# Kernel tuning notes

Measured on AMD Instinct MI355X. Metric: run time of the kernel, lower is better.

## Reference

```python
import jax, jax.numpy as jnp
import numpy as np

TOP_K = 2

def setup_inputs() -> dict:
    key = jax.random.key(0)
    kx, kg, k1, k2 = jax.random.split(key, 4)
    B, T, D, E, H = 4, 1024, 1024, 8, 2048
    x = jax.random.normal(kx, (B, T, D), dtype=jnp.float32)
    Wg = jax.random.normal(kg, (D, E), dtype=jnp.float32) * 0.02
    W1 = jax.random.normal(k1, (E, D, H), dtype=jnp.float32) * 0.02  # c_fc per expert
    W2 = jax.random.normal(k2, (E, H, D), dtype=jnp.float32) * 0.02  # c_proj per expert
    return {"x": x, "Wg": Wg, "W1": W1, "W2": W2}

def reference(x, Wg, W1, W2):
    B, T, D = x.shape
    E = W1.shape[0]
    # Router: softmax over experts, top-k, renormalize top-k weights
    logits = jnp.einsum('btd,de->bte', x, Wg)          # (B,T,E)
    probs = jax.nn.softmax(logits, axis=-1)
    top_w, top_i = jax.lax.top_k(probs, TOP_K)          # (B,T,K)
    top_w = top_w / (jnp.sum(top_w, axis=-1, keepdims=True) + 1e-8)
    # Combine weights per (token, expert): sum_k top_w[k] * one_hot(top_i[k])
    N = B * T
    oh = jax.nn.one_hot(top_i.reshape(N, TOP_K), E, dtype=x.dtype)   # (N,K,E)
    combine = jnp.sum(oh * top_w.reshape(N, TOP_K)[..., None], axis=1)  # (N,E)
    # Expert MLPs: relu(x W1)^2 W2, evaluated densely and combined (same math)
    xt = x.reshape(N, D)
    h = jnp.einsum('td,edh->teh', xt, W1)               # (N,E,H)
    h = jnp.square(jax.nn.relu(h))
    y = jnp.einsum('teh,ehd->ted', h, W2)               # (N,E,D)
    out = jnp.einsum('te,ted->td', combine, y)          # (N,D)
    return out.reshape(B, T, D)
```

## Files before the change

### kernel.cpp

```cpp
#include <hip/hip_runtime.h>
#include <hip/hip_bf16.h>
#include <stdint.h>

#define NTOK 4096
#define DD 1024
#define EE 8
#define HH 2048
#define BM 128
#define BN 128
#define BK 64
#define MAXRB 72
#define RPAD (MAXRB*BM)

typedef __attribute__((ext_vector_type(4))) float f32x4;
typedef __attribute__((ext_vector_type(8))) short bf16x8;

__device__ __forceinline__ void gload16(const void* g, void* l) {
  __builtin_amdgcn_global_load_lds((const __attribute__((address_space(1))) unsigned int*)g,
                                   (__attribute__((address_space(3))) unsigned int*)l, 16, 0, 0);
}

__global__ __launch_bounds__(256) void router_kernel(const float* __restrict__ x,
    const float* __restrict__ Wg, double* __restrict__ logitsD) {
  int t = blockIdx.x;
  int tid = threadIdx.x;
  const float* xr = x + (size_t)t * DD;
  double acc[EE];
  #pragma unroll
  for (int e = 0; e < EE; ++e) acc[e] = 0.0;
  #pragma unroll
  for (int i = 0; i < DD/256; ++i) {
    int d = tid + i*256;
    float xv = xr[d];
    float4 w0 = *(const float4*)(Wg + (size_t)d*EE);
    float4 w1 = *(const float4*)(Wg + (size_t)d*EE + 4);
    double xd = (double)xv;
    acc[0] += xd * (double)w0.x; acc[1] += xd * (double)w0.y;
    acc[2] += xd * (double)w0.z; acc[3] += xd * (double)w0.w;
    acc[4] += xd * (double)w1.x; acc[5] += xd * (double)w1.y;
    acc[6] += xd * (double)w1.z; acc[7] += xd * (double)w1.w;
  }
  #pragma unroll
  for (int e = 0; e < EE; ++e) {
    double v = acc[e];
    #pragma unroll
    for (int off = 32; off > 0; off >>= 1) v += __shfl_down(v, off, 64);
    acc[e] = v;
  }
  __shared__ double sAcc[4][EE];
  int lane = tid & 63, w = tid >> 6;
  if (lane == 0) {
    #pragma unroll
    for (int e = 0; e < EE; ++e) sAcc[w][e] = acc[e];
  }
  __syncthreads();
  if (tid < EE)
    logitsD[(size_t)t*EE + tid] = sAcc[0][tid] + sAcc[1][tid] + sAcc[2][tid] + sAcc[3][tid];
}

__global__ __launch_bounds__(256) void softtop_kernel(const double* __restrict__ logitsD,
    int* __restrict__ topE, float* __restrict__ topW, int* __restrict__ counts) {
  __shared__ int hist[EE];
  if (threadIdx.x < EE) hist[threadIdx.x] = 0;
  __syncthreads();
  int t = blockIdx.x * 256 + threadIdx.x;
  double s[EE];
  #pragma unroll
  for (int e = 0; e < EE; ++e) s[e] = logitsD[(size_t)t*EE + e];
  double mx = s[0];
  #pragma unroll
  for (int e = 1; e < EE; ++e) mx = fmax(mx, s[e]);
  double p[EE], Z = 0.0;
  #pragma unroll
  for (int e = 0; e < EE; ++e) { p[e] = exp(s[e] - mx); Z += p[e]; }
  #pragma unroll
  for (int e = 0; e < EE; ++e) p[e] /= Z;
  int i0 = 0;
  #pragma unroll
  for (int e = 1; e < EE; ++e) if (p[e] > p[i0]) i0 = e;
  int i1 = -1;
  #pragma unroll
  for (int e = 0; e < EE; ++e) { if (e == i0) continue; if (i1 < 0 || p[e] > p[i1]) i1 = e; }
  double sm = p[i0] + p[i1] + 1e-8;
  topE[t*2]   = i0; topE[t*2+1] = i1;
  topW[t*2]   = (float)(p[i0] / sm);
  topW[t*2+1] = (float)(p[i1] / sm);
  atomicAdd(&hist[i0], 1); atomicAdd(&hist[i1], 1);
  __syncthreads();
  if (threadIdx.x < EE) atomicAdd(&counts[threadIdx.x], hist[threadIdx.x]);
}

__global__ void setup_kernel(const int* __restrict__ counts, int* __restrict__ po,
                             int* __restrict__ nRB, int* __restrict__ rbExpert,
                             int* __restrict__ pairsTok) {
  if (threadIdx.x == 0) {
    int off = 0;
    for (int e = 0; e < EE; ++e) {
      po[e] = off;
      off += ((counts[e] + BM - 1) / BM) * BM;
    }
    po[EE] = off;
    *nRB = off / BM;
    int rb = 0;
    for (int e = 0; e < EE; ++e) {
      int nb = (((counts[e] + BM - 1) / BM));
      for (int b = 0; b < nb; ++b) rbExpert[rb++] = e;
    }
  }
  __syncthreads();
  for (int i = threadIdx.x; i < RPAD; i += blockDim.x) pairsTok[i] = -1;
}

__global__ __launch_bounds__(1024) void assign_kernel(const int* __restrict__ topE,
    const float* __restrict__ topW, const int* __restrict__ po,
    int* __restrict__ pairsTok, float* __restrict__ pairsW, int* __restrict__ slotOf) {
  __shared__ int base[EE];
  __shared__ int wcnt[16][EE];
  int tid = threadIdx.x, wv = tid >> 6, lane = tid & 63;
  if (tid < EE) base[tid] = po[tid];
  __syncthreads();
  for (int it = 0; it < 2*NTOK/1024; ++it) {
    int p = it*1024 + tid;
    int e = topE[p];
    int myrank = 0;
    #pragma unroll
    for (int ee = 0; ee < EE; ++ee) {
      unsigned long long b = __ballot(e == ee);
      if (ee == e) myrank = __popcll(b & ((1ull << lane) - 1ull));
      if (lane == 0) wcnt[wv][ee] = __popcll(b);
    }
    __syncthreads();
    int wbase = 0;
    for (int w2 = 0; w2 < wv; ++w2) wbase += wcnt[w2][e];
    int slot = base[e] + wbase + myrank;
    pairsTok[slot] = p >> 1;
    pairsW[slot]   = topW[p];
    slotOf[p]      = slot;
    __syncthreads();
    if (tid < EE) {
      int s2 = 0;
      #pragma unroll
      for (int w2 = 0; w2 < 16; ++w2) s2 += wcnt[w2][tid];
      base[tid] += s2;
    }
    __syncthreads();
  }
}

__global__ __launch_bounds__(256) void gather_kernel(const float* __restrict__ x,
    const int* __restrict__ slotOf, __hip_bfloat16* __restrict__ Xg) {
  int t = blockIdx.x;
  int s0 = slotOf[2*t], s1 = slotOf[2*t+1];
  const float* xr = x + (size_t)t * DD;
  int i = threadIdx.x;
  float4 v = ((const float4*)xr)[i];
  ushort4 b;
  b.x = __bfloat16_as_ushort(__float2bfloat16(v.x));
  b.y = __bfloat16_as_ushort(__float2bfloat16(v.y));
  b.z = __bfloat16_as_ushort(__float2bfloat16(v.z));
  b.w = __bfloat16_as_ushort(__float2bfloat16(v.w));
  ((ushort4*)(Xg + (size_t)s0 * DD))[i] = b;
  ((ushort4*)(Xg + (size_t)s1 * DD))[i] = b;
}

__global__ __launch_bounds__(256) void transpose_conv_kernel(const float* __restrict__ in,
    __hip_bfloat16* __restrict__ out, int R, int C) {
  __shared__ float tile[64][65];
  int tilesC = C >> 6;
  int tilesPerE = (R >> 6) * tilesC;
  int b = blockIdx.x;
  int e = b / tilesPerE;
  int rem = b % tilesPerE;
  int tr = rem / tilesC, tc = rem % tilesC;
  const float* src = in + (size_t)e * R * C + (size_t)(tr*64) * C + tc*64;
  int col = threadIdx.x & 63;
  int row0 = threadIdx.x >> 6;
  #pragma unroll
  for (int i = 0; i < 16; ++i) {
    int r = row0 + i*4;
    tile[r][col] = src[(size_t)r * C + col];
  }
  __syncthreads();
  __hip_bfloat16* dst = out + (size_t)e * R * C + (size_t)(tc*64) * R + tr*64;
  #pragma unroll
  for (int i = 0; i < 16; ++i) {
    int r = row0 + i*4;
    dst[(size_t)r * R + col] = __float2bfloat16(tile[col][r]);
  }
}

template<int EPI, int KDIM, int NTOT>
__global__ __launch_bounds__(256)
void gemm_kernel(const __hip_bfloat16* __restrict__ A,
                 const __hip_bfloat16* __restrict__ Ball,
                 __hip_bfloat16* __restrict__ Cbf,
                 float* __restrict__ Cf,
                 const int* __restrict__ nRB,
                 const int* __restrict__ rbExpert,
                 const int* __restrict__ pairsTok,
                 const float* __restrict__ pairsW) {
  int rb = blockIdx.x;
  if (rb >= *nRB) return;
  int nb = blockIdx.y;
  int e = rbExpert[rb];
  const __hip_bfloat16* Ag = A + (size_t)rb * BM * KDIM;
  const __hip_bfloat16* Bg = Ball + (size_t)e * NTOT * KDIM + (size_t)nb * BN * KDIM;
  __shared__ __align__(16) __hip_bfloat16 As[BM*BK];
  __shared__ __align__(16) __hip_bfloat16 Bs[BN*BK];
  __shared__ int   sTok[BM];
  __shared__ float sW[BM];
  int tid = threadIdx.x;
  if (EPI == 1 && tid < BM) {
    sTok[tid] = pairsTok[rb*BM + tid];
    sW[tid]   = pairsW[rb*BM + tid];
  }
  int lane = tid & 63;
  int wid = tid >> 6;
  int wr = wid >> 1, wc = wid & 1;
  int l15 = lane & 15;
  int lhi = lane >> 4;
  f32x4 acc[4][4] = {};
  int srow  = tid >> 3;
  int scol8 = (tid & 7) * 8;
  for (int kt = 0; kt < KDIM / BK; ++kt) {
    #pragma unroll
    for (int i = 0; i < 4; ++i) {
      int r = srow + 32*i;
      int sc = scol8 ^ ((r & 7) << 3);
      gload16(Ag + (size_t)r * KDIM + kt*BK + sc, (char*)As + i*4096 + tid*16);
      gload16(Bg + (size_t)r * KDIM + kt*BK + sc, (char*)Bs + i*4096 + tid*16);
    }
    __syncthreads();
    #pragma unroll
    for (int kk = 0; kk < 2; ++kk) {
      bf16x8 af[4], bfr[4];
      int kb = kk*64 + lhi*16;
      #pragma unroll
      for (int m = 0; m < 4; ++m) {
        int row = wr*64 + m*16 + l15;
        af[m] = *(const bf16x8*)((const char*)As + row*128 + (kb ^ ((row & 7) << 4)));
      }
      #pragma unroll
      for (int n = 0; n < 4; ++n) {
        int row = wc*64 + n*16 + l15;
        bfr[n] = *(const bf16x8*)((const char*)Bs + row*128 + (kb ^ ((row & 7) << 4)));
      }
      #pragma unroll
      for (int m = 0; m < 4; ++m)
        #pragma unroll
        for (int n = 0; n < 4; ++n)
          acc[m][n] = __builtin_amdgcn_mfma_f32_16x16x32_bf16(af[m], bfr[n], acc[m][n], 0, 0, 0);
    }
    __syncthreads();
  }
  if (EPI == 0) {
    #pragma unroll
    for (int m = 0; m < 4; ++m) {
      int row = rb*BM + wr*64 + m*16 + lhi*4;
      #pragma unroll
      for (int n = 0; n < 4; ++n) {
        int col = nb*BN + wc*64 + n*16 + l15;
        #pragma unroll
        for (int j = 0; j < 4; ++j) {
          float v = fmaxf(acc[m][n][j], 0.0f);
          Cbf[(size_t)(row + j) * NTOT + col] = __float2bfloat16(v * v);
        }
      }
    }
  } else {
    #pragma unroll
    for (int m = 0; m < 4; ++m) {
      int rloc = wr*64 + m*16 + lhi*4;
      #pragma unroll
      for (int j = 0; j < 4; ++j) {
        int tok = sTok[rloc + j];
        if (tok < 0) continue;
        float w = sW[rloc + j];
        #pragma unroll
        for (int n = 0; n < 4; ++n) {
          int col = nb*BN + wc*64 + n*16 + l15;
          atomicAdd(Cf + (size_t)tok * NTOT + col, w * acc[m][n][j]);
        }
      }
    }
  }
}


extern "C" void kernel_launch(void* const* d_in, const int* in_sizes, int n_in,
                              void* d_out, int out_size, void* d_ws, size_t ws_size,
                              hipStream_t stream) {
  const float* x  = (const float*)d_in[0];
  const float* Wg = (const float*)d_in[1];
  const float* W1 = (const float*)d_in[2];
  const float* W2 = (const float*)d_in[3];
  float* out = (float*)d_out;
  char* ws = (char*)d_ws;

  int*   counts   = (int*)(ws + 0);
  int*   po       = (int*)(ws + 128);
  int*   nRB      = (int*)(ws + 192);
  int*   rbExpert = (int*)(ws + 256);
  int*   topE     = (int*)(ws + 1024);
  float* topW     = (float*)(ws + 40960);
  int*   pairsTok = (int*)(ws + 73728);
  float* pairsW   = (float*)(ws + 110592);
  int*   slotOf   = (int*)(ws + 147456);
  __hip_bfloat16* Xg   = (__hip_bfloat16*)(ws + 262144);
  __hip_bfloat16* Hbuf = (__hip_bfloat16*)(ws + 19136512);
  double* logitsD = (double*)(ws + 19136512);
  __hip_bfloat16* W1bT = (__hip_bfloat16*)(ws + 56885248);
  __hip_bfloat16* W2bT = (__hip_bfloat16*)(ws + 90439680);

  hipMemsetAsync(d_out, 0, (size_t)out_size * sizeof(float), stream);
  hipMemsetAsync(ws, 0, 128, stream);

  router_kernel<<<NTOK, 256, 0, stream>>>(x, Wg, logitsD);
  softtop_kernel<<<NTOK/256, 256, 0, stream>>>(logitsD, topE, topW, counts);
  setup_kernel<<<1, 256, 0, stream>>>(counts, po, nRB, rbExpert, pairsTok);
  assign_kernel<<<1, 1024, 0, stream>>>(topE, topW, po, pairsTok, pairsW, slotOf);
  gather_kernel<<<NTOK, 256, 0, stream>>>(x, slotOf, Xg);
  transpose_conv_kernel<<<EE*(DD/64)*(HH/64), 256, 0, stream>>>(W1, W1bT, DD, HH);
  transpose_conv_kernel<<<EE*(HH/64)*(DD/64), 256, 0, stream>>>(W2, W2bT, HH, DD);

  gemm_kernel<0, DD, HH><<<dim3(MAXRB, HH/BN), 256, 0, stream>>>(
      Xg, W1bT, Hbuf, nullptr, nRB, rbExpert, pairsTok, pairsW);
  gemm_kernel<1, HH, DD><<<dim3(MAXRB, DD/BN), 256, 0, stream>>>(
      Hbuf, W2bT, nullptr, out, nRB, rbExpert, pairsTok, pairsW);
}
```

Before: 223.2 us.

## Double-buffer GEMM LDS, remap blocks per XCD, vectorize weight transpose, merge setup

The GEMM kernels now double-buffer the A/B LDS tiles so the global-to-LDS loads for the next k-tile are issued while the current tile is multiplied. They also use a 1D grid remapped so each XCD handles a contiguous group of 9 row blocks, which is meant to improve L2 reuse of expert weights. The weight transpose/convert kernel now reads float4, converts to bf16 before storing to LDS, and writes 16-byte vectors. The setup kernel is merged into the assign kernel to drop one launch. Double buffering doubles LDS use per block, which may reduce occupancy.

```diff
diff --git a/kernel.cpp b/kernel.cpp
--- a/kernel.cpp
+++ b/kernel.cpp
@@ -90,10 +90,14 @@
   if (threadIdx.x < EE) atomicAdd(&counts[threadIdx.x], hist[threadIdx.x]);
 }
 
-__global__ void setup_kernel(const int* __restrict__ counts, int* __restrict__ po,
-                             int* __restrict__ nRB, int* __restrict__ rbExpert,
-                             int* __restrict__ pairsTok) {
-  if (threadIdx.x == 0) {
+__global__ __launch_bounds__(1024) void assign_kernel(const int* __restrict__ counts,
+    const int* __restrict__ topE, const float* __restrict__ topW,
+    int* __restrict__ po, int* __restrict__ nRB, int* __restrict__ rbExpert,
+    int* __restrict__ pairsTok, float* __restrict__ pairsW, int* __restrict__ slotOf) {
+  __shared__ int base[EE];
+  __shared__ int wcnt[16][EE];
+  int tid = threadIdx.x, wv = tid >> 6, lane = tid & 63;
+  if (tid == 0) {
     int off = 0;
     for (int e = 0; e < EE; ++e) {
       po[e] = off;
@@ -103,20 +107,12 @@
     *nRB = off / BM;
     int rb = 0;
     for (int e = 0; e < EE; ++e) {
-      int nb = (((counts[e] + BM - 1) / BM));
+      int nb = (counts[e] + BM - 1) / BM;
       for (int b = 0; b < nb; ++b) rbExpert[rb++] = e;
     }
   }
-  __syncthreads();
-  for (int i = threadIdx.x; i < RPAD; i += blockDim.x) pairsTok[i] = -1;
-}
-
-__global__ __launch_bounds__(1024) void assign_kernel(const int* __restrict__ topE,
-    const float* __restrict__ topW, const int* __restrict__ po,
-    int* __restrict__ pairsTok, float* __restrict__ pairsW, int* __restrict__ slotOf) {
-  __shared__ int base[EE];
-  __shared__ int wcnt[16][EE];
-  int tid = threadIdx.x, wv = tid >> 6, lane = tid & 63;
+  for (int i = tid; i < RPAD; i += 1024) pairsTok[i] = -1;
+  __syncthreads();
   if (tid < EE) base[tid] = po[tid];
   __syncthreads();
   for (int it = 0; it < 2*NTOK/1024; ++it) {
@@ -165,7 +161,7 @@
 
 __global__ __launch_bounds__(256) void transpose_conv_kernel(const float* __restrict__ in,
     __hip_bfloat16* __restrict__ out, int R, int C) {
-  __shared__ float tile[64][65];
+  __shared__ __hip_bfloat16 tile[64][70];
   int tilesC = C >> 6;
   int tilesPerE = (R >> 6) * tilesC;
   int b = blockIdx.x;
@@ -173,20 +169,30 @@
   int rem = b % tilesPerE;
   int tr = rem / tilesC, tc = rem % tilesC;
   const float* src = in + (size_t)e * R * C + (size_t)(tr*64) * C + tc*64;
-  int col = threadIdx.x & 63;
-  int row0 = threadIdx.x >> 6;
-  #pragma unroll
-  for (int i = 0; i < 16; ++i) {
-    int r = row0 + i*4;
-    tile[r][col] = src[(size_t)r * C + col];
+  int rr = threadIdx.x >> 4;
+  int c4 = (threadIdx.x & 15) << 2;
+  #pragma unroll
+  for (int i = 0; i < 4; ++i) {
+    int r = rr + (i << 4);
+    float4 v = *(const float4*)(src + (size_t)r * C + c4);
+    ushort4 u;
+    u.x = __bfloat16_as_ushort(__float2bfloat16(v.x));
+    u.y = __bfloat16_as_ushort(__float2bfloat16(v.y));
+    u.z = __bfloat16_as_ushort(__float2bfloat16(v.z));
+    u.w = __bfloat16_as_ushort(__float2bfloat16(v.w));
+    *(ushort4*)&tile[r][c4] = u;
   }
   __syncthreads();
   __hip_bfloat16* dst = out + (size_t)e * R * C + (size_t)(tc*64) * R + tr*64;
-  #pragma unroll
-  for (int i = 0; i < 16; ++i) {
-    int r = row0 + i*4;
-    dst[(size_t)r * R + col] = __float2bfloat16(tile[col][r]);
-  }
+  int orow = threadIdx.x >> 2;
+  int seg  = (threadIdx.x & 3) << 4;
+  bf16x8 w0, w1;
+  #pragma unroll
+  for (int j = 0; j < 8; ++j) w0[j] = (short)__bfloat16_as_ushort(tile[seg + j][orow]);
+  #pragma unroll
+  for (int j = 0; j < 8; ++j) w1[j] = (short)__bfloat16_as_ushort(tile[seg + 8 + j][orow]);
+  *(bf16x8*)(dst + (size_t)orow * R + seg)     = w0;
+  *(bf16x8*)(dst + (size_t)orow * R + seg + 8) = w1;
 }
 
 template<int EPI, int KDIM, int NTOT>
@@ -199,14 +205,17 @@
                  const int* __restrict__ rbExpert,
                  const int* __restrict__ pairsTok,
                  const float* __restrict__ pairsW) {
-  int rb = blockIdx.x;
+  int bid = blockIdx.x;
+  int xcd = bid & 7;
+  int slot = bid >> 3;
+  int rb = xcd * 9 + (slot % 9);
+  int nb = slot / 9;
   if (rb >= *nRB) return;
-  int nb = blockIdx.y;
   int e = rbExpert[rb];
   const __hip_bfloat16* Ag = A + (size_t)rb * BM * KDIM;
   const __hip_bfloat16* Bg = Ball + (size_t)e * NTOT * KDIM + (size_t)nb * BN * KDIM;
-  __shared__ __align__(16) __hip_bfloat16 As[BM*BK];
-  __shared__ __align__(16) __hip_bfloat16 Bs[BN*BK];
+  __shared__ __align__(16) __hip_bfloat16 As[2][BM*BK];
+  __shared__ __align__(16) __hip_bfloat16 Bs[2][BN*BK];
   __shared__ int   sTok[BM];
   __shared__ float sW[BM];
   int tid = threadIdx.x;
@@ -222,15 +231,22 @@
   f32x4 acc[4][4] = {};
   int srow  = tid >> 3;
   int scol8 = (tid & 7) * 8;
-  for (int kt = 0; kt < KDIM / BK; ++kt) {
-    #pragma unroll
-    for (int i = 0; i < 4; ++i) {
-      int r = srow + 32*i;
-      int sc = scol8 ^ ((r & 7) << 3);
-      gload16(Ag + (size_t)r * KDIM + kt*BK + sc, (char*)As + i*4096 + tid*16);
-      gload16(Bg + (size_t)r * KDIM + kt*BK + sc, (char*)Bs + i*4096 + tid*16);
-    }
-    __syncthreads();
+
+  #define STAGE(buf, kt) {                                                      \
+    _Pragma("unroll")                                                           \
+    for (int i = 0; i < 4; ++i) {                                               \
+      int r = srow + 32*i;                                                      \
+      int sc = scol8 ^ ((r & 7) << 3);                                          \
+      gload16(Ag + (size_t)r * KDIM + (kt)*BK + sc, (char*)&As[buf][0] + i*4096 + tid*16); \
+      gload16(Bg + (size_t)r * KDIM + (kt)*BK + sc, (char*)&Bs[buf][0] + i*4096 + tid*16); \
+    } }
+
+  constexpr int NT = KDIM / BK;
+  STAGE(0, 0);
+  __syncthreads();
+  int cur = 0;
+  for (int kt = 0; kt < NT; ++kt) {
+    if (kt + 1 < NT) STAGE(cur ^ 1, kt + 1);
     #pragma unroll
     for (int kk = 0; kk < 2; ++kk) {
       bf16x8 af[4], bfr[4];
@@ -238,12 +254,12 @@
       #pragma unroll
       for (int m = 0; m < 4; ++m) {
         int row = wr*64 + m*16 + l15;
-        af[m] = *(const bf16x8*)((const char*)As + row*128 + (kb ^ ((row & 7) << 4)));
+        af[m] = *(const bf16x8*)((const char*)&As[cur][0] + row*128 + (kb ^ ((row & 7) << 4)));
       }
       #pragma unroll
       for (int n = 0; n < 4; ++n) {
         int row = wc*64 + n*16 + l15;
-        bfr[n] = *(const bf16x8*)((const char*)Bs + row*128 + (kb ^ ((row & 7) << 4)));
+        bfr[n] = *(const bf16x8*)((const char*)&Bs[cur][0] + row*128 + (kb ^ ((row & 7) << 4)));
       }
       #pragma unroll
       for (int m = 0; m < 4; ++m)
@@ -252,7 +268,10 @@
           acc[m][n] = __builtin_amdgcn_mfma_f32_16x16x32_bf16(af[m], bfr[n], acc[m][n], 0, 0, 0);
     }
     __syncthreads();
-  }
+    cur ^= 1;
+  }
+  #undef STAGE
+
   if (EPI == 0) {
     #pragma unroll
     for (int m = 0; m < 4; ++m) {
@@ -317,14 +336,14 @@
 
   router_kernel<<<NTOK, 256, 0, stream>>>(x, Wg, logitsD);
   softtop_kernel<<<NTOK/256, 256, 0, stream>>>(logitsD, topE, topW, counts);
-  setup_kernel<<<1, 256, 0, stream>>>(counts, po, nRB, rbExpert, pairsTok);
-  assign_kernel<<<1, 1024, 0, stream>>>(topE, topW, po, pairsTok, pairsW, slotOf);
+  assign_kernel<<<1, 1024, 0, stream>>>(counts, topE, topW, po, nRB, rbExpert,
+                                        pairsTok, pairsW, slotOf);
   gather_kernel<<<NTOK, 256, 0, stream>>>(x, slotOf, Xg);
   transpose_conv_kernel<<<EE*(DD/64)*(HH/64), 256, 0, stream>>>(W1, W1bT, DD, HH);
   transpose_conv_kernel<<<EE*(HH/64)*(DD/64), 256, 0, stream>>>(W2, W2bT, HH, DD);
 
-  gemm_kernel<0, DD, HH><<<dim3(MAXRB, HH/BN), 256, 0, stream>>>(
+  gemm_kernel<0, DD, HH><<<MAXRB*(HH/BN), 256, 0, stream>>>(
       Xg, W1bT, Hbuf, nullptr, nRB, rbExpert, pairsTok, pairsW);
-  gemm_kernel<1, HH, DD><<<dim3(MAXRB, DD/BN), 256, 0, stream>>>(
+  gemm_kernel<1, HH, DD><<<MAXRB*(DD/BN), 256, 0, stream>>>(
       Hbuf, W2bT, nullptr, out, nRB, rbExpert, pairsTok, pairsW);
 }
```

Measured after the change: 246.7 us. +10.5%, slower.
